# Kernel tuning notes

Hardware: AMD Instinct MI355X
Metric: run time of the kernel (lower is better)

Reference implementation:

```python
import jax, jax.numpy as jnp
import numpy as np

INPUT_SIZE = 12288  # C*H*W = 3*64*64
HIDDEN = 1024
OUT_SHAPE = (3, 64, 64)
T_STEPS = 256


def setup_inputs() -> dict:
    key = jax.random.key(0)
    ks = jax.random.split(key, 7)
    s = 0.02
    frames = jax.random.normal(ks[0], (T_STEPS, *OUT_SHAPE), dtype=jnp.float32)
    W_ih = jax.random.normal(ks[1], (4 * HIDDEN, INPUT_SIZE), dtype=jnp.float32) * s
    W_hh = jax.random.normal(ks[2], (4 * HIDDEN, HIDDEN), dtype=jnp.float32) * s
    b_ih = jax.random.normal(ks[3], (4 * HIDDEN,), dtype=jnp.float32) * s
    b_hh = jax.random.normal(ks[4], (4 * HIDDEN,), dtype=jnp.float32) * s
    fc_w = jax.random.normal(ks[5], (INPUT_SIZE, HIDDEN), dtype=jnp.float32) * s
    fc_b = jax.random.normal(ks[6], (INPUT_SIZE,), dtype=jnp.float32) * s
    return {"frames": frames, "W_ih": W_ih, "W_hh": W_hh, "b_ih": b_ih,
            "b_hh": b_hh, "fc_w": fc_w, "fc_b": fc_b, "T": T_STEPS}


def _lstm_scan(x_flat, W_ih, W_hh, b_ih, b_hh):
    # Precompute input projections for all timesteps in one GEMM: (T, 4H)
    x_proj = x_flat @ W_ih.T + b_ih + b_hh
    H = W_hh.shape[1]

    def step(carry, xp):
        h, c = carry  # (H,), (H,)
        gates = xp + h @ W_hh.T  # (4H,)
        i = jax.nn.sigmoid(gates[0 * H:1 * H])
        f = jax.nn.sigmoid(gates[1 * H:2 * H])
        g = jnp.tanh(gates[2 * H:3 * H])
        o = jax.nn.sigmoid(gates[3 * H:4 * H])
        c_new = f * c + i * g
        h_new = o * jnp.tanh(c_new)
        return (h_new, c_new), None

    init = (jnp.zeros((H,), x_flat.dtype), jnp.zeros((H,), x_flat.dtype))
    (h_T, _), _ = jax.lax.scan(step, init, x_proj)
    return h_T


def reference(frames, W_ih, W_hh, b_ih, b_hh, fc_w, fc_b, T):
    Tn, C, Hh, Ww = frames.shape
    x_flat = frames.reshape(Tn, -1)  # (T, C*H*W)
    h_T = _lstm_scan(x_flat, W_ih, W_hh, b_ih, b_hh)  # (HIDDEN,)
    context = h_T @ fc_w.T + fc_b  # (C*H*W,)
    return context.reshape(1, C, Hh, Ww)
```

## Files before the change

kernel.cpp:

```cpp
#include <hip/hip_runtime.h>
#include <math.h>

#define K_IN 12288
#define HID  1024
#define G4   4096
#define TS   256

typedef unsigned long long u64;
typedef unsigned int u32;
typedef __attribute__((ext_vector_type(4))) float f32x4;
typedef __attribute__((ext_vector_type(16))) float f32x16;
typedef __attribute__((ext_vector_type(8))) _Float16 half8;
typedef __attribute__((ext_vector_type(4))) _Float16 half4;

__global__ __launch_bounds__(512, 2) void xproj_gemm(
    const float* __restrict__ X,
    const float* __restrict__ W,
    float* __restrict__ xpartT,
    int kspan)
{
  __shared__ __align__(16) _Float16 Ahi[2][128][8];
  __shared__ __align__(16) _Float16 Alo[2][128][8];
  __shared__ __align__(16) _Float16 Bhi[2][256][8];
  __shared__ __align__(16) _Float16 Blo[2][256][8];

  const int tid = threadIdx.x;
  const int wave = tid >> 6;
  const int lane = tid & 63;
  const int l31 = lane & 31;
  const int kh = lane >> 5;

  const int j0 = blockIdx.x * 128;
  const int ks = blockIdx.y;
  const int kbeg = ks * kspan;

  const int jw = (wave & 1) * 64;
  const int tw = (wave >> 1) * 64;

  const int wrow = tid >> 2;
  const int wkq  = tid & 3;
  const int xrow = tid >> 1;
  const int xkq  = tid & 1;

  const float* wsrc = W + (size_t)(j0 + wrow) * K_IN + kbeg + wkq * 4;
  const float* xsrc = X + (size_t)xrow * K_IN + kbeg + xkq * 8;

  f32x16 acc[2][2];
#pragma unroll
  for (int mi = 0; mi < 2; ++mi)
#pragma unroll
    for (int ni = 0; ni < 2; ++ni)
#pragma unroll
      for (int e = 0; e < 16; ++e) acc[mi][ni][e] = 0.f;

  f32x4 wv  = *(const f32x4*)wsrc;
  f32x4 xv0 = *(const f32x4*)xsrc;
  f32x4 xv1 = *(const f32x4*)(xsrc + 4);

  const int nsteps = kspan >> 4;
  for (int s = 0; s < nsteps; ++s) {
    {
      half4 hw, lw;
#pragma unroll
      for (int e = 0; e < 4; ++e) {
        _Float16 h = (_Float16)wv[e];
        hw[e] = h;
        lw[e] = (_Float16)(wv[e] - (float)h);
      }
      *(half4*)&Ahi[wkq >> 1][wrow][(wkq & 1) * 4] = hw;
      *(half4*)&Alo[wkq >> 1][wrow][(wkq & 1) * 4] = lw;
      half8 hx, lx;
#pragma unroll
      for (int e = 0; e < 4; ++e) {
        _Float16 h0 = (_Float16)xv0[e];
        hx[e] = h0;
        lx[e] = (_Float16)(xv0[e] - (float)h0);
        _Float16 h1 = (_Float16)xv1[e];
        hx[e + 4] = h1;
        lx[e + 4] = (_Float16)(xv1[e] - (float)h1);
      }
      *(half8*)&Bhi[xkq][xrow][0] = hx;
      *(half8*)&Blo[xkq][xrow][0] = lx;
    }
    __syncthreads();

    if (s + 1 < nsteps) {
      const int ko = (s + 1) * 16;
      wv  = *(const f32x4*)(wsrc + ko);
      xv0 = *(const f32x4*)(xsrc + ko);
      xv1 = *(const f32x4*)(xsrc + ko + 4);
    }

    half8 aH[2], aL[2], bH[2], bL[2];
#pragma unroll
    for (int mi = 0; mi < 2; ++mi) {
      aH[mi] = *(const half8*)&Ahi[kh][jw + mi * 32 + l31][0];
      aL[mi] = *(const half8*)&Alo[kh][jw + mi * 32 + l31][0];
    }
#pragma unroll
    for (int ni = 0; ni < 2; ++ni) {
      bH[ni] = *(const half8*)&Bhi[kh][tw + ni * 32 + l31][0];
      bL[ni] = *(const half8*)&Blo[kh][tw + ni * 32 + l31][0];
    }

    acc[0][0] = __builtin_amdgcn_mfma_f32_32x32x16_f16(aH[0], bH[0], acc[0][0], 0, 0, 0);
    acc[0][1] = __builtin_amdgcn_mfma_f32_32x32x16_f16(aH[0], bH[1], acc[0][1], 0, 0, 0);
    acc[1][0] = __builtin_amdgcn_mfma_f32_32x32x16_f16(aH[1], bH[0], acc[1][0], 0, 0, 0);
    acc[1][1] = __builtin_amdgcn_mfma_f32_32x32x16_f16(aH[1], bH[1], acc[1][1], 0, 0, 0);
    acc[0][0] = __builtin_amdgcn_mfma_f32_32x32x16_f16(aH[0], bL[0], acc[0][0], 0, 0, 0);
    acc[0][1] = __builtin_amdgcn_mfma_f32_32x32x16_f16(aH[0], bL[1], acc[0][1], 0, 0, 0);
    acc[1][0] = __builtin_amdgcn_mfma_f32_32x32x16_f16(aH[1], bL[0], acc[1][0], 0, 0, 0);
    acc[1][1] = __builtin_amdgcn_mfma_f32_32x32x16_f16(aH[1], bL[1], acc[1][1], 0, 0, 0);
    acc[0][0] = __builtin_amdgcn_mfma_f32_32x32x16_f16(aL[0], bH[0], acc[0][0], 0, 0, 0);
    acc[0][1] = __builtin_amdgcn_mfma_f32_32x32x16_f16(aL[0], bH[1], acc[0][1], 0, 0, 0);
    acc[1][0] = __builtin_amdgcn_mfma_f32_32x32x16_f16(aL[1], bH[0], acc[1][0], 0, 0, 0);
    acc[1][1] = __builtin_amdgcn_mfma_f32_32x32x16_f16(aL[1], bH[1], acc[1][1], 0, 0, 0);

    __syncthreads();
  }

  float* outp = xpartT + (size_t)ks * G4 * TS;
#pragma unroll
  for (int mi = 0; mi < 2; ++mi)
#pragma unroll
    for (int ni = 0; ni < 2; ++ni)
#pragma unroll
      for (int rg = 0; rg < 16; ++rg) {
        const int j = j0 + jw + mi * 32 + (rg & 3) + 8 * (rg >> 2) + 4 * kh;
        const int t = tw + ni * 32 + l31;
        outp[(size_t)j * TS + t] = acc[mi][ni][rg];
      }
}

__global__ __launch_bounds__(256) void xproj_reduce(
    const float* __restrict__ xpartT, int nks,
    const float* __restrict__ b_ih, const float* __restrict__ b_hh,
    float* __restrict__ xprojT)
{
  const int idx = (blockIdx.x * 256 + threadIdx.x) * 4;
  float4 s = *(const float4*)(xpartT + idx);
  for (int ks = 1; ks < nks; ++ks) {
    float4 p = *(const float4*)(xpartT + (size_t)ks * G4 * TS + idx);
    s.x += p.x; s.y += p.y; s.z += p.z; s.w += p.w;
  }
  const int j = idx >> 8;
  const float bias = b_ih[j] + b_hh[j];
  s.x += bias; s.y += bias; s.z += bias; s.w += bias;
  *(float4*)(xprojT + idx) = s;
}

#define NWG 128
#define UPW 8

__global__ __launch_bounds__(256, 1) void lstm_scan(
    const float* __restrict__ W_hh,
    const float* __restrict__ xprojT,
    u64* __restrict__ hmsg)
{
  const int tid = threadIdx.x;
  const int w = blockIdx.x;
  const int u0 = w * UPW;
  const int r = tid >> 3;
  const int sub = tid & 7;
  const int gate = r >> 3;
  const int uu = r & 7;
  const int hrow = gate * HID + u0 + uu;

  __shared__ __align__(16) float h_lds[8 * 132];
  __shared__ float gates_lds[32];
  __shared__ float c_lds[UPW];

  float4 Wreg[32];
  const float4* wp = (const float4*)(W_hh + (size_t)hrow * HID + sub * 128);
#pragma unroll
  for (int i = 0; i < 32; ++i) Wreg[i] = wp[i];

  const float* xrow = xprojT + (size_t)hrow * TS;

  if (tid < UPW) c_lds[tid] = 0.f;
  __syncthreads();

  for (int t = 0; t < TS; ++t) {
    float xp = 0.f;
    if (sub == 0) xp = xrow[t];

    float partial = 0.f;
    if (t > 0) {
      const u64* slot = hmsg + (t & 1) * HID;
      const u32 tt = (u32)t;
      u64 m0, m1, m2, m3;
      do {
        m0 = __hip_atomic_load(&slot[tid * 4 + 0], __ATOMIC_RELAXED,
                               __HIP_MEMORY_SCOPE_AGENT);
      } while ((u32)(m0 >> 32) != tt);
      m1 = __hip_atomic_load(&slot[tid * 4 + 1], __ATOMIC_RELAXED,
                             __HIP_MEMORY_SCOPE_AGENT);
      m2 = __hip_atomic_load(&slot[tid * 4 + 2], __ATOMIC_RELAXED,
                             __HIP_MEMORY_SCOPE_AGENT);
      m3 = __hip_atomic_load(&slot[tid * 4 + 3], __ATOMIC_RELAXED,
                             __HIP_MEMORY_SCOPE_AGENT);
      while ((u32)(m1 >> 32) != tt)
        m1 = __hip_atomic_load(&slot[tid * 4 + 1], __ATOMIC_RELAXED,
                               __HIP_MEMORY_SCOPE_AGENT);
      while ((u32)(m2 >> 32) != tt)
        m2 = __hip_atomic_load(&slot[tid * 4 + 2], __ATOMIC_RELAXED,
                               __HIP_MEMORY_SCOPE_AGENT);
      while ((u32)(m3 >> 32) != tt)
        m3 = __hip_atomic_load(&slot[tid * 4 + 3], __ATOMIC_RELAXED,
                               __HIP_MEMORY_SCOPE_AGENT);
      __syncthreads();
      const int st = tid >> 5;
      const int off = (tid & 31) * 4;
      h_lds[st * 132 + off + 0] = __uint_as_float((u32)m0);
      h_lds[st * 132 + off + 1] = __uint_as_float((u32)m1);
      h_lds[st * 132 + off + 2] = __uint_as_float((u32)m2);
      h_lds[st * 132 + off + 3] = __uint_as_float((u32)m3);
      __syncthreads();
      const float4* hl = (const float4*)(h_lds + sub * 132);
#pragma unroll
      for (int i = 0; i < 32; ++i) {
        float4 h4 = hl[i];
        partial += Wreg[i].x * h4.x + Wreg[i].y * h4.y +
                   Wreg[i].z * h4.z + Wreg[i].w * h4.w;
      }
    }
    partial += __shfl_xor(partial, 1, 64);
    partial += __shfl_xor(partial, 2, 64);
    partial += __shfl_xor(partial, 4, 64);
    if (sub == 0) {
      float gsum = partial + xp;
      float act = (gate == 2) ? tanhf(gsum) : 1.f / (1.f + expf(-gsum));
      gates_lds[gate * 8 + uu] = act;
    }
    __syncthreads();
    if (tid < UPW) {
      float iv = gates_lds[0 * 8 + tid];
      float fv = gates_lds[1 * 8 + tid];
      float gv = gates_lds[2 * 8 + tid];
      float ov = gates_lds[3 * 8 + tid];
      float c = fv * c_lds[tid] + iv * gv;
      c_lds[tid] = c;
      float hnew = ov * tanhf(c);
      u64 msg = ((u64)(u32)(t + 1) << 32) | (u64)__float_as_uint(hnew);
      __hip_atomic_store(&hmsg[((t + 1) & 1) * HID + u0 + tid], msg,
                         __ATOMIC_RELAXED, __HIP_MEMORY_SCOPE_AGENT);
    }
  }
}

__global__ __launch_bounds__(256) void fc_kernel(
    const float* __restrict__ fc_w,
    const float* __restrict__ fc_b,
    const u64* __restrict__ hmsg,
    float* __restrict__ out)
{
  __shared__ float h_s[HID];
  const int tid = threadIdx.x;
  for (int k = tid; k < HID; k += 256)
    h_s[k] = __uint_as_float((u32)hmsg[k]);
  __syncthreads();
  const int r = tid >> 2;
  const int sub = tid & 3;
  const int j = blockIdx.x * 64 + r;
  const float4* wrow = (const float4*)(fc_w + (size_t)j * HID + sub * 256);
  const float4* hp = (const float4*)(h_s + sub * 256);
  float s = 0.f;
#pragma unroll
  for (int i = 0; i < 64; ++i) {
    float4 wv = wrow[i];
    float4 hv = hp[i];
    s += wv.x * hv.x + wv.y * hv.y + wv.z * hv.z + wv.w * hv.w;
  }
  s += __shfl_xor(s, 1, 64);
  s += __shfl_xor(s, 2, 64);
  if (sub == 0) out[j] = s + fc_b[j];
}

extern "C" void kernel_launch(void* const* d_in, const int* in_sizes, int n_in,
                              void* d_out, int out_size, void* d_ws, size_t ws_size,
                              hipStream_t stream) {
  const float* frames = (const float*)d_in[0];
  const float* W_ih   = (const float*)d_in[1];
  const float* W_hh   = (const float*)d_in[2];
  const float* b_ih   = (const float*)d_in[3];
  const float* b_hh   = (const float*)d_in[4];
  const float* fc_w   = (const float*)d_in[5];
  const float* fc_b   = (const float*)d_in[6];
  float* out = (float*)d_out;

  const size_t XPROJ_BYTES = (size_t)TS * G4 * 4;
  int nks = 1;
  if (ws_size >= XPROJ_BYTES * 9 + (1 << 20)) nks = 8;
  else if (ws_size >= XPROJ_BYTES * 5 + (1 << 20)) nks = 4;
  else if (ws_size >= XPROJ_BYTES * 3 + (1 << 20)) nks = 2;

  char* ws = (char*)d_ws;
  float* xprojT = (float*)ws;
  float* xpartT = (float*)(ws + XPROJ_BYTES);
  u64*   hmsg   = (u64*)(ws + XPROJ_BYTES * (1 + nks));

  const int kspan = K_IN / nks;
  xproj_gemm<<<dim3(G4 / 128, nks), 512, 0, stream>>>(frames, W_ih, xpartT, kspan);
  xproj_reduce<<<dim3(G4 * TS / 4 / 256), 256, 0, stream>>>(xpartT, nks, b_ih, b_hh, xprojT);
  lstm_scan<<<dim3(NWG), 256, 0, stream>>>(W_hh, xprojT, hmsg);
  fc_kernel<<<dim3(12288 / 64), 256, 0, stream>>>(fc_w, fc_b, hmsg, out);
}
```

Baseline: 1.023 ms.

## Replace split-K partial buffers and reduce kernel with atomic accumulation

The separate split-K reduction kernel goes away. The GEMM now atomically adds its partial tiles into a zeroed xproj buffer, and the bias add moves into the LSTM scan kernel. The GEMM main loop is unrolled by two with double register prefetch, and the recurrent dot product uses four independent accumulators to shorten the FMA dependency chain. This saves the partial-buffer traffic and one launch, at the cost of a memset, float atomics, and a nondeterministic summation order.

```diff
diff --git a/kernel.cpp b/kernel.cpp
--- a/kernel.cpp
+++ b/kernel.cpp
@@ -5,6 +5,9 @@
 #define HID  1024
 #define G4   4096
 #define TS   256
+#define NKS  8
+#define KSP  (K_IN / NKS)
+#define NST  (KSP / 16)
 
 typedef unsigned long long u64;
 typedef unsigned int u32;
@@ -16,8 +19,7 @@
 __global__ __launch_bounds__(512, 2) void xproj_gemm(
     const float* __restrict__ X,
     const float* __restrict__ W,
-    float* __restrict__ xpartT,
-    int kspan)
+    float* __restrict__ xprojT)
 {
   __shared__ __align__(16) _Float16 Ahi[2][128][8];
   __shared__ __align__(16) _Float16 Alo[2][128][8];
@@ -31,8 +33,7 @@
   const int kh = lane >> 5;
 
   const int j0 = blockIdx.x * 128;
-  const int ks = blockIdx.y;
-  const int kbeg = ks * kspan;
+  const int kbeg = blockIdx.y * KSP;
 
   const int jw = (wave & 1) * 64;
   const int tw = (wave >> 1) * 64;
@@ -53,73 +54,88 @@
 #pragma unroll
       for (int e = 0; e < 16; ++e) acc[mi][ni][e] = 0.f;
 
-  f32x4 wv  = *(const f32x4*)wsrc;
-  f32x4 xv0 = *(const f32x4*)xsrc;
-  f32x4 xv1 = *(const f32x4*)(xsrc + 4);
-
-  const int nsteps = kspan >> 4;
-  for (int s = 0; s < nsteps; ++s) {
-    {
-      half4 hw, lw;
-#pragma unroll
-      for (int e = 0; e < 4; ++e) {
-        _Float16 h = (_Float16)wv[e];
-        hw[e] = h;
-        lw[e] = (_Float16)(wv[e] - (float)h);
-      }
-      *(half4*)&Ahi[wkq >> 1][wrow][(wkq & 1) * 4] = hw;
-      *(half4*)&Alo[wkq >> 1][wrow][(wkq & 1) * 4] = lw;
-      half8 hx, lx;
-#pragma unroll
-      for (int e = 0; e < 4; ++e) {
-        _Float16 h0 = (_Float16)xv0[e];
-        hx[e] = h0;
-        lx[e] = (_Float16)(xv0[e] - (float)h0);
-        _Float16 h1 = (_Float16)xv1[e];
-        hx[e + 4] = h1;
-        lx[e + 4] = (_Float16)(xv1[e] - (float)h1);
-      }
-      *(half8*)&Bhi[xkq][xrow][0] = hx;
-      *(half8*)&Blo[xkq][xrow][0] = lx;
-    }
-    __syncthreads();
-
-    if (s + 1 < nsteps) {
-      const int ko = (s + 1) * 16;
-      wv  = *(const f32x4*)(wsrc + ko);
-      xv0 = *(const f32x4*)(xsrc + ko);
-      xv1 = *(const f32x4*)(xsrc + ko + 4);
-    }
-
-    half8 aH[2], aL[2], bH[2], bL[2];
-#pragma unroll
-    for (int mi = 0; mi < 2; ++mi) {
-      aH[mi] = *(const half8*)&Ahi[kh][jw + mi * 32 + l31][0];
-      aL[mi] = *(const half8*)&Alo[kh][jw + mi * 32 + l31][0];
-    }
-#pragma unroll
-    for (int ni = 0; ni < 2; ++ni) {
-      bH[ni] = *(const half8*)&Bhi[kh][tw + ni * 32 + l31][0];
-      bL[ni] = *(const half8*)&Blo[kh][tw + ni * 32 + l31][0];
-    }
-
-    acc[0][0] = __builtin_amdgcn_mfma_f32_32x32x16_f16(aH[0], bH[0], acc[0][0], 0, 0, 0);
-    acc[0][1] = __builtin_amdgcn_mfma_f32_32x32x16_f16(aH[0], bH[1], acc[0][1], 0, 0, 0);
-    acc[1][0] = __builtin_amdgcn_mfma_f32_32x32x16_f16(aH[1], bH[0], acc[1][0], 0, 0, 0);
-    acc[1][1] = __builtin_amdgcn_mfma_f32_32x32x16_f16(aH[1], bH[1], acc[1][1], 0, 0, 0);
-    acc[0][0] = __builtin_amdgcn_mfma_f32_32x32x16_f16(aH[0], bL[0], acc[0][0], 0, 0, 0);
-    acc[0][1] = __builtin_amdgcn_mfma_f32_32x32x16_f16(aH[0], bL[1], acc[0][1], 0, 0, 0);
-    acc[1][0] = __builtin_amdgcn_mfma_f32_32x32x16_f16(aH[1], bL[0], acc[1][0], 0, 0, 0);
-    acc[1][1] = __builtin_amdgcn_mfma_f32_32x32x16_f16(aH[1], bL[1], acc[1][1], 0, 0, 0);
-    acc[0][0] = __builtin_amdgcn_mfma_f32_32x32x16_f16(aL[0], bH[0], acc[0][0], 0, 0, 0);
-    acc[0][1] = __builtin_amdgcn_mfma_f32_32x32x16_f16(aL[0], bH[1], acc[0][1], 0, 0, 0);
-    acc[1][0] = __builtin_amdgcn_mfma_f32_32x32x16_f16(aL[1], bH[0], acc[1][0], 0, 0, 0);
-    acc[1][1] = __builtin_amdgcn_mfma_f32_32x32x16_f16(aL[1], bH[1], acc[1][1], 0, 0, 0);
-
-    __syncthreads();
-  }
-
-  float* outp = xpartT + (size_t)ks * G4 * TS;
+  f32x4 wvA  = *(const f32x4*)(wsrc);
+  f32x4 xv0A = *(const f32x4*)(xsrc);
+  f32x4 xv1A = *(const f32x4*)(xsrc + 4);
+  f32x4 wvB  = *(const f32x4*)(wsrc + 16);
+  f32x4 xv0B = *(const f32x4*)(xsrc + 16);
+  f32x4 xv1B = *(const f32x4*)(xsrc + 16 + 4);
+
+#define STAGE(WV, XV0, XV1)                                                  \
+  {                                                                          \
+    half4 hw, lw;                                                            \
+    _Pragma("unroll")                                                        \
+    for (int e = 0; e < 4; ++e) {                                            \
+      _Float16 h = (_Float16)WV[e];                                          \
+      hw[e] = h;                                                             \
+      lw[e] = (_Float16)(WV[e] - (float)h);                                  \
+    }                                                                        \
+    *(half4*)&Ahi[wkq >> 1][wrow][(wkq & 1) * 4] = hw;                       \
+    *(half4*)&Alo[wkq >> 1][wrow][(wkq & 1) * 4] = lw;                       \
+    half8 hx, lx;                                                            \
+    _Pragma("unroll")                                                        \
+    for (int e = 0; e < 4; ++e) {                                            \
+      _Float16 h0 = (_Float16)XV0[e];                                        \
+      hx[e] = h0;                                                            \
+      lx[e] = (_Float16)(XV0[e] - (float)h0);                                \
+      _Float16 h1 = (_Float16)XV1[e];                                        \
+      hx[e + 4] = h1;                                                        \
+      lx[e + 4] = (_Float16)(XV1[e] - (float)h1);                            \
+    }                                                                        \
+    *(half8*)&Bhi[xkq][xrow][0] = hx;                                        \
+    *(half8*)&Blo[xkq][xrow][0] = lx;                                        \
+  }
+
+#define COMPUTE()                                                            \
+  {                                                                          \
+    half8 aH[2], aL[2], bH[2], bL[2];                                        \
+    _Pragma("unroll")                                                        \
+    for (int mi = 0; mi < 2; ++mi) {                                         \
+      aH[mi] = *(const half8*)&Ahi[kh][jw + mi * 32 + l31][0];               \
+      aL[mi] = *(const half8*)&Alo[kh][jw + mi * 32 + l31][0];               \
+    }                                                                        \
+    _Pragma("unroll")                                                        \
+    for (int ni = 0; ni < 2; ++ni) {                                         \
+      bH[ni] = *(const half8*)&Bhi[kh][tw + ni * 32 + l31][0];               \
+      bL[ni] = *(const half8*)&Blo[kh][tw + ni * 32 + l31][0];               \
+    }                                                                        \
+    acc[0][0] = __builtin_amdgcn_mfma_f32_32x32x16_f16(aH[0], bH[0], acc[0][0], 0, 0, 0); \
+    acc[0][1] = __builtin_amdgcn_mfma_f32_32x32x16_f16(aH[0], bH[1], acc[0][1], 0, 0, 0); \
+    acc[1][0] = __builtin_amdgcn_mfma_f32_32x32x16_f16(aH[1], bH[0], acc[1][0], 0, 0, 0); \
+    acc[1][1] = __builtin_amdgcn_mfma_f32_32x32x16_f16(aH[1], bH[1], acc[1][1], 0, 0, 0); \
+    acc[0][0] = __builtin_amdgcn_mfma_f32_32x32x16_f16(aH[0], bL[0], acc[0][0], 0, 0, 0); \
+    acc[0][1] = __builtin_amdgcn_mfma_f32_32x32x16_f16(aH[0], bL[1], acc[0][1], 0, 0, 0); \
+    acc[1][0] = __builtin_amdgcn_mfma_f32_32x32x16_f16(aH[1], bL[0], acc[1][0], 0, 0, 0); \
+    acc[1][1] = __builtin_amdgcn_mfma_f32_32x32x16_f16(aH[1], bL[1], acc[1][1], 0, 0, 0); \
+    acc[0][0] = __builtin_amdgcn_mfma_f32_32x32x16_f16(aL[0], bH[0], acc[0][0], 0, 0, 0); \
+    acc[0][1] = __builtin_amdgcn_mfma_f32_32x32x16_f16(aL[0], bH[1], acc[0][1], 0, 0, 0); \
+    acc[1][0] = __builtin_amdgcn_mfma_f32_32x32x16_f16(aL[1], bH[0], acc[1][0], 0, 0, 0); \
+    acc[1][1] = __builtin_amdgcn_mfma_f32_32x32x16_f16(aL[1], bH[1], acc[1][1], 0, 0, 0); \
+  }
+
+  for (int s = 0; s < NST; s += 2) {
+    STAGE(wvA, xv0A, xv1A);
+    __syncthreads();
+    if (s + 2 < NST) {
+      const int ko = (s + 2) * 16;
+      wvA  = *(const f32x4*)(wsrc + ko);
+      xv0A = *(const f32x4*)(xsrc + ko);
+      xv1A = *(const f32x4*)(xsrc + ko + 4);
+    }
+    COMPUTE();
+    __syncthreads();
+    STAGE(wvB, xv0B, xv1B);
+    __syncthreads();
+    if (s + 3 < NST) {
+      const int ko = (s + 3) * 16;
+      wvB  = *(const f32x4*)(wsrc + ko);
+      xv0B = *(const f32x4*)(xsrc + ko);
+      xv1B = *(const f32x4*)(xsrc + ko + 4);
+    }
+    COMPUTE();
+    __syncthreads();
+  }
+
 #pragma unroll
   for (int mi = 0; mi < 2; ++mi)
 #pragma unroll
@@ -128,25 +144,8 @@
       for (int rg = 0; rg < 16; ++rg) {
         const int j = j0 + jw + mi * 32 + (rg & 3) + 8 * (rg >> 2) + 4 * kh;
         const int t = tw + ni * 32 + l31;
-        outp[(size_t)j * TS + t] = acc[mi][ni][rg];
+        atomicAdd(&xprojT[(size_t)j * TS + t], acc[mi][ni][rg]);
       }
-}
-
-__global__ __launch_bounds__(256) void xproj_reduce(
-    const float* __restrict__ xpartT, int nks,
-    const float* __restrict__ b_ih, const float* __restrict__ b_hh,
-    float* __restrict__ xprojT)
-{
-  const int idx = (blockIdx.x * 256 + threadIdx.x) * 4;
-  float4 s = *(const float4*)(xpartT + idx);
-  for (int ks = 1; ks < nks; ++ks) {
-    float4 p = *(const float4*)(xpartT + (size_t)ks * G4 * TS + idx);
-    s.x += p.x; s.y += p.y; s.z += p.z; s.w += p.w;
-  }
-  const int j = idx >> 8;
-  const float bias = b_ih[j] + b_hh[j];
-  s.x += bias; s.y += bias; s.z += bias; s.w += bias;
-  *(float4*)(xprojT + idx) = s;
 }
 
 #define NWG 128
@@ -155,6 +154,7 @@
 __global__ __launch_bounds__(256, 1) void lstm_scan(
     const float* __restrict__ W_hh,
     const float* __restrict__ xprojT,
+    const float* __restrict__ b_ih, const float* __restrict__ b_hh,
     u64* __restrict__ hmsg)
 {
   const int tid = threadIdx.x;
@@ -176,15 +176,16 @@
   for (int i = 0; i < 32; ++i) Wreg[i] = wp[i];
 
   const float* xrow = xprojT + (size_t)hrow * TS;
+  const float bias = b_ih[hrow] + b_hh[hrow];
 
   if (tid < UPW) c_lds[tid] = 0.f;
   __syncthreads();
 
   for (int t = 0; t < TS; ++t) {
     float xp = 0.f;
-    if (sub == 0) xp = xrow[t];
-
-    float partial = 0.f;
+    if (sub == 0) xp = xrow[t] + bias;
+
+    float p0 = 0.f, p1 = 0.f, p2 = 0.f, p3 = 0.f;
     if (t > 0) {
       const u64* slot = hmsg + (t & 1) * HID;
       const u32 tt = (u32)t;
@@ -218,12 +219,23 @@
       __syncthreads();
       const float4* hl = (const float4*)(h_lds + sub * 132);
 #pragma unroll
-      for (int i = 0; i < 32; ++i) {
-        float4 h4 = hl[i];
-        partial += Wreg[i].x * h4.x + Wreg[i].y * h4.y +
-                   Wreg[i].z * h4.z + Wreg[i].w * h4.w;
+      for (int i = 0; i < 32; i += 4) {
+        float4 h4;
+        h4 = hl[i + 0];
+        p0 += Wreg[i + 0].x * h4.x + Wreg[i + 0].y * h4.y +
+              Wreg[i + 0].z * h4.z + Wreg[i + 0].w * h4.w;
+        h4 = hl[i + 1];
+        p1 += Wreg[i + 1].x * h4.x + Wreg[i + 1].y * h4.y +
+              Wreg[i + 1].z * h4.z + Wreg[i + 1].w * h4.w;
+        h4 = hl[i + 2];
+        p2 += Wreg[i + 2].x * h4.x + Wreg[i + 2].y * h4.y +
+              Wreg[i + 2].z * h4.z + Wreg[i + 2].w * h4.w;
+        h4 = hl[i + 3];
+        p3 += Wreg[i + 3].x * h4.x + Wreg[i + 3].y * h4.y +
+              Wreg[i + 3].z * h4.z + Wreg[i + 3].w * h4.w;
       }
     }
+    float partial = (p0 + p1) + (p2 + p3);
     partial += __shfl_xor(partial, 1, 64);
     partial += __shfl_xor(partial, 2, 64);
     partial += __shfl_xor(partial, 4, 64);
@@ -289,19 +301,12 @@
   float* out = (float*)d_out;
 
   const size_t XPROJ_BYTES = (size_t)TS * G4 * 4;
-  int nks = 1;
-  if (ws_size >= XPROJ_BYTES * 9 + (1 << 20)) nks = 8;
-  else if (ws_size >= XPROJ_BYTES * 5 + (1 << 20)) nks = 4;
-  else if (ws_size >= XPROJ_BYTES * 3 + (1 << 20)) nks = 2;
-
   char* ws = (char*)d_ws;
   float* xprojT = (float*)ws;
-  float* xpartT = (float*)(ws + XPROJ_BYTES);
-  u64*   hmsg   = (u64*)(ws + XPROJ_BYTES * (1 + nks));
-
-  const int kspan = K_IN / nks;
-  xproj_gemm<<<dim3(G4 / 128, nks), 512, 0, stream>>>(frames, W_ih, xpartT, kspan);
-  xproj_reduce<<<dim3(G4 * TS / 4 / 256), 256, 0, stream>>>(xpartT, nks, b_ih, b_hh, xprojT);
-  lstm_scan<<<dim3(NWG), 256, 0, stream>>>(W_hh, xprojT, hmsg);
+  u64*   hmsg   = (u64*)(ws + XPROJ_BYTES);
+
+  hipMemsetAsync(xprojT, 0, XPROJ_BYTES, stream);
+  xproj_gemm<<<dim3(G4 / 128, NKS), 512, 0, stream>>>(frames, W_ih, xprojT);
+  lstm_scan<<<dim3(NWG), 256, 0, stream>>>(W_hh, xprojT, b_ih, b_hh, hmsg);
   fc_kernel<<<dim3(12288 / 64), 256, 0, stream>>>(fc_w, fc_b, hmsg, out);
 }
```

Measured after the change: 1.083 ms. 5.9% more time.
